# Kernel optimization log

Measured on AMD Instinct MI355X. Metric: run time of the kernel, lower is better.

The kernel has to match this reference:

```python
import jax, jax.numpy as jnp
import numpy as np

D = 256
NODE_COUNTS = [200000, 50000, 12000, 4000]  # n_src per block; dst of block l = NODE_COUNTS[l+1]
EDGE_COUNTS = [500000, 120000, 40000]


def setup_inputs() -> dict:
    key = jax.random.key(0)
    ks = jax.random.split(key, 16)
    x = jax.random.normal(ks[0], (NODE_COUNTS[0], D), dtype=jnp.float32)
    inp = {"x": x}
    scale = 1.0 / np.sqrt(D)
    ki = 1
    for l in range(3):
        inp[f"Wself{l}"] = jax.random.normal(ks[ki], (D, D), dtype=jnp.float32) * scale; ki += 1
        inp[f"Wneigh{l}"] = jax.random.normal(ks[ki], (D, D), dtype=jnp.float32) * scale; ki += 1
        inp[f"b{l}"] = jnp.zeros((D,), dtype=jnp.float32)
    for l in range(3):
        e = EDGE_COUNTS[l]
        inp[f"src{l}"] = jax.random.randint(ks[ki], (e,), 0, NODE_COUNTS[l]); ki += 1
        inp[f"dst{l}"] = jax.random.randint(ks[ki], (e,), 0, NODE_COUNTS[l + 1]); ki += 1
    inp["nd0"], inp["nd1"], inp["nd2"] = NODE_COUNTS[1], NODE_COUNTS[2], NODE_COUNTS[3]
    return inp


def _sage_layer(h, src, dst, n_dst, Ws, Wn, b, relu=True):
    # DGL SAGEConv('mean'): out = fc_self(h_dst) + fc_neigh(mean_{u in N(v)} h_u) + bias
    h_dst = h[:n_dst]
    msgs = h[src]                                               # [E, d] gather
    agg = jax.ops.segment_sum(msgs, dst, num_segments=n_dst)    # [n_dst, d]
    deg = jax.ops.segment_sum(jnp.ones((dst.shape[0],), h.dtype), dst, num_segments=n_dst)
    mean = agg / jnp.maximum(deg, 1.0)[:, None]
    out = h_dst @ Ws + mean @ Wn + b
    return jax.nn.relu(out) if relu else out


def reference(x, Wself0, Wneigh0, b0, Wself1, Wneigh1, b1, Wself2, Wneigh2, b2,
              src0, dst0, src1, dst1, src2, dst2, nd0, nd1, nd2):
    h = _sage_layer(x, src0, dst0, nd0, Wself0, Wneigh0, b0)
    h = _sage_layer(h, src1, dst1, nd1, Wself1, Wneigh1, b1)
    h = _sage_layer(h, src2, dst2, nd2, Wself2, Wneigh2, b2)
    return h
```

## Files before the change

kernel.cpp:

```cpp
#include <hip/hip_runtime.h>
#include <stdint.h>

#define D 256

typedef __attribute__((ext_vector_type(8))) short bf16x8;
typedef __attribute__((ext_vector_type(4))) float f32x4;

__device__ inline unsigned short f2bf(float f) {
    union { float f; uint32_t u; } v; v.f = f;
    return (unsigned short)((v.u + 0x7FFFu + ((v.u >> 16) & 1u)) >> 16);
}
__device__ inline float bf2f(unsigned short b) {
    return __uint_as_float(((uint32_t)b) << 16);
}

#define SEG0 0
#define SEG1 50176
#define SEG2 62464
#define CURTOT 66560
#define NBLK 65

#define WBLK 1536
#define XBLK 25000

struct PreArgs {
    const float* w[6];
    const float* x;
    unsigned short* wt;
    unsigned short* xb;
    const int* d0; const int* d1; const int* d2;
    int* cur;
    int E0, E01, Etot, cblk0;
};

__global__ __launch_bounds__(256) void fused_pre(PreArgs a)
{
    int b = blockIdx.x;
    if (b < WBLK) {
        int t = b * 256 + threadIdx.x;
        int m = t >> 16, e = t & 65535;
        int col = e >> 8, k = e & 255;
        a.wt[t] = f2bf(a.w[m][(k << 8) + col]);
    } else if (b < WBLK + XBLK) {
        long t = (long)(b - WBLK) * 256 + threadIdx.x;
        const float4* p = (const float4*)a.x + t * 2;
        float4 v0 = p[0], v1 = p[1];
        unsigned short r[8] = {f2bf(v0.x), f2bf(v0.y), f2bf(v0.z), f2bf(v0.w),
                               f2bf(v1.x), f2bf(v1.y), f2bf(v1.z), f2bf(v1.w)};
        *(uint4*)(a.xb + t * 8) = *(uint4*)r;
    } else {
        int e = (b - a.cblk0) * 256 + threadIdx.x;
        if (e >= a.Etot) return;
        int base, d;
        if (e < a.E0)       { base = SEG0; d = a.d0[e]; }
        else if (e < a.E01) { base = SEG1; d = a.d1[e - a.E0]; }
        else                { base = SEG2; d = a.d2[e - a.E01]; }
        atomicAdd(&a.cur[base + d], 1);
    }
}

__global__ __launch_bounds__(256) void scan_blocks(
    int* __restrict__ cur, int* __restrict__ bsum)
{
    __shared__ int wsum[4];
    int tid = threadIdx.x, lane = tid & 63, wid = tid >> 6;
    int base = blockIdx.x * 1024 + tid * 4;
    int4 v = *(int4*)(cur + base);
    int t0 = v.x, t01 = t0 + v.y, t012 = t01 + v.z, tot = t012 + v.w;
    int incl = tot;
    #pragma unroll
    for (int ofs = 1; ofs < 64; ofs <<= 1) {
        int t = __shfl_up(incl, ofs, 64);
        if (lane >= ofs) incl += t;
    }
    if (lane == 63) wsum[wid] = incl;
    __syncthreads();
    if (tid == 0) {
        int run = 0;
        #pragma unroll
        for (int w = 0; w < 4; ++w) { int t = wsum[w]; wsum[w] = run; run += t; }
        bsum[blockIdx.x] = run;
    }
    __syncthreads();
    int texcl = wsum[wid] + incl - tot;
    v.x = texcl; v.y = texcl + t0; v.z = texcl + t01; v.w = texcl + t012;
    *(int4*)(cur + base) = v;
}

__global__ __launch_bounds__(128) void scan_bsums(
    const int* __restrict__ bsum, int* __restrict__ bscan)
{
    __shared__ int s[NBLK];
    int tid = threadIdx.x;
    if (tid < NBLK) s[tid] = bsum[tid];
    __syncthreads();
    if (tid == 0) {
        int run = 0;
        for (int b = 0; b < 49; ++b)  { int t = s[b]; s[b] = run; run += t; }
        run = 0;
        for (int b = 49; b < 61; ++b) { int t = s[b]; s[b] = run; run += t; }
        run = 0;
        for (int b = 61; b < 65; ++b) { int t = s[b]; s[b] = run; run += t; }
    }
    __syncthreads();
    if (tid < NBLK) bscan[tid] = s[tid];
}

__global__ __launch_bounds__(256) void scan_addback(
    int* __restrict__ cur, const int* __restrict__ bscan)
{
    int base = blockIdx.x * 1024 + threadIdx.x * 4;
    int add = bscan[blockIdx.x];
    int4 v = *(int4*)(cur + base);
    v.x += add; v.y += add; v.z += add; v.w += add;
    *(int4*)(cur + base) = v;
}

__global__ __launch_bounds__(256) void fill_all(
    const int* __restrict__ s0, const int* __restrict__ s1, const int* __restrict__ s2,
    const int* __restrict__ d0, const int* __restrict__ d1, const int* __restrict__ d2,
    int* __restrict__ cur, int* __restrict__ idx, int E0, int E01, int Etot)
{
    int e = blockIdx.x * 256 + threadIdx.x;
    if (e >= Etot) return;
    int base, d, s, ib;
    if (e < E0)       { base = SEG0; d = d0[e];       s = s0[e];       ib = 0; }
    else if (e < E01) { base = SEG1; d = d1[e - E0];  s = s1[e - E0];  ib = E0; }
    else              { base = SEG2; d = d2[e - E01]; s = s2[e - E01]; ib = E01; }
    int p = atomicAdd(&cur[base + d], 1);
    idx[ib + p] = s;
}

__global__ __launch_bounds__(256) void gather_mean_k(
    const unsigned short* __restrict__ h, const int* __restrict__ idx,
    const int* __restrict__ curseg, unsigned short* __restrict__ mean, int M)
{
    int t = blockIdx.x * blockDim.x + threadIdx.x;
    int w = t >> 6, lane = t & 63;
    if (w >= M) return;
    int e0 = w ? curseg[w - 1] : 0;
    int e1 = curseg[w];
    float4 acc = make_float4(0.f, 0.f, 0.f, 0.f);
    int e = e0;
    for (; e + 1 < e1; e += 2) {
        int sa = idx[e], sb = idx[e + 1];
        ushort4 va = *(const ushort4*)(h + (size_t)sa * D + lane * 4);
        ushort4 vb = *(const ushort4*)(h + (size_t)sb * D + lane * 4);
        acc.x += bf2f(va.x) + bf2f(vb.x);
        acc.y += bf2f(va.y) + bf2f(vb.y);
        acc.z += bf2f(va.z) + bf2f(vb.z);
        acc.w += bf2f(va.w) + bf2f(vb.w);
    }
    if (e < e1) {
        int sa = idx[e];
        ushort4 va = *(const ushort4*)(h + (size_t)sa * D + lane * 4);
        acc.x += bf2f(va.x); acc.y += bf2f(va.y);
        acc.z += bf2f(va.z); acc.w += bf2f(va.w);
    }
    float r = 1.0f / fmaxf((float)(e1 - e0), 1.0f);
    ushort4 o;
    o.x = f2bf(acc.x * r); o.y = f2bf(acc.y * r);
    o.z = f2bf(acc.z * r); o.w = f2bf(acc.w * r);
    *(ushort4*)(mean + (size_t)w * D + lane * 4) = o;
}

template<int FINAL>
__global__ __launch_bounds__(256, 2) void sage_gemm_mfma(
    const unsigned short* __restrict__ A1,
    const unsigned short* __restrict__ A2,
    const unsigned short* __restrict__ Wt1,
    const unsigned short* __restrict__ Wt2,
    const float* __restrict__ bias,
    void* __restrict__ outv,
    int M)
{
    __shared__ unsigned short As[128 * 32];
    __shared__ unsigned short Bs[256 * 32];

    int tid = threadIdx.x;
    int lane = tid & 63, wid = tid >> 6;
    int wr = wid >> 1, wc = wid & 1;
    int m0 = blockIdx.x * 128;
    int l15 = lane & 15, lq = lane >> 4;

    f32x4 acc[4][8] = {};

    for (int kt = 0; kt < 16; ++kt) {
        const unsigned short* A = (kt < 8) ? A1 : A2;
        const unsigned short* B = (kt < 8) ? Wt1 : Wt2;
        int kk = (kt & 7) * 32;
        #pragma unroll
        for (int q = 0; q < 2; ++q) {
            int ch = q * 256 + tid;
            int r = ch >> 2, c16 = ch & 3;
            int gr = m0 + r; if (gr >= M) gr = M - 1;
            const unsigned short* src = A + (size_t)gr * 256 + kk + c16 * 8;
            __builtin_amdgcn_global_load_lds(
                (const __attribute__((address_space(1))) void*)src,
                (__attribute__((address_space(3))) void*)(As + (q * 256 + wid * 64) * 8),
                16, 0, 0);
        }
        #pragma unroll
        for (int q = 0; q < 4; ++q) {
            int ch = q * 256 + tid;
            int col = ch >> 2, c16 = ch & 3;
            const unsigned short* src = B + (size_t)col * 256 + kk + c16 * 8;
            __builtin_amdgcn_global_load_lds(
                (const __attribute__((address_space(1))) void*)src,
                (__attribute__((address_space(3))) void*)(Bs + (q * 256 + wid * 64) * 8),
                16, 0, 0);
        }
        __syncthreads();

        bf16x8 af[4], bfr[8];
        #pragma unroll
        for (int i = 0; i < 4; ++i)
            af[i] = *(const bf16x8*)(As + (wr * 64 + i * 16 + l15) * 32 + lq * 8);
        #pragma unroll
        for (int i = 0; i < 8; ++i)
            bfr[i] = *(const bf16x8*)(Bs + (wc * 128 + i * 16 + l15) * 32 + lq * 8);

        #pragma unroll
        for (int mr = 0; mr < 4; ++mr)
            #pragma unroll
            for (int nc = 0; nc < 8; ++nc)
                acc[mr][nc] = __builtin_amdgcn_mfma_f32_16x16x32_bf16(
                    af[mr], bfr[nc], acc[mr][nc], 0, 0, 0);
        __syncthreads();
    }

    #pragma unroll
    for (int nc = 0; nc < 8; ++nc) {
        int gc = wc * 128 + nc * 16 + l15;
        float bv = bias[gc];
        #pragma unroll
        for (int mr = 0; mr < 4; ++mr) {
            #pragma unroll
            for (int reg = 0; reg < 4; ++reg) {
                int gr = m0 + wr * 64 + mr * 16 + lq * 4 + reg;
                if (gr < M) {
                    float v = fmaxf(acc[mr][nc][reg] + bv, 0.f);
                    if (FINAL) ((float*)outv)[(size_t)gr * 256 + gc] = v;
                    else ((unsigned short*)outv)[(size_t)gr * 256 + gc] = f2bf(v);
                }
            }
        }
    }
}

extern "C" void kernel_launch(void* const* d_in, const int* in_sizes, int n_in,
                              void* d_out, int out_size, void* d_ws, size_t ws_size,
                              hipStream_t stream) {
    const float* x = (const float*)d_in[0];
    const float* Wself[3]  = {(const float*)d_in[1], (const float*)d_in[4], (const float*)d_in[7]};
    const float* Wneigh[3] = {(const float*)d_in[2], (const float*)d_in[5], (const float*)d_in[8]};
    const float* bias[3]   = {(const float*)d_in[3], (const float*)d_in[6], (const float*)d_in[9]};
    const int* src[3] = {(const int*)d_in[10], (const int*)d_in[12], (const int*)d_in[14]};
    const int* dst[3] = {(const int*)d_in[11], (const int*)d_in[13], (const int*)d_in[15]};
    int E[3]    = {in_sizes[10], in_sizes[12], in_sizes[14]};
    int ndst[3] = {50000, 12000, 4000};
    int E0 = E[0], E01 = E[0] + E[1], Etot = E[0] + E[1] + E[2];

    unsigned short* xb    = (unsigned short*)d_ws;
    unsigned short* h1b   = xb + (size_t)200000 * D;
    unsigned short* h2b   = h1b + (size_t)50000 * D;
    unsigned short* meanb = h2b + (size_t)12000 * D;
    unsigned short* wt    = meanb + (size_t)50000 * D;
    int* cur   = (int*)(wt + 6 * 65536);
    int* bsum  = cur + CURTOT;
    int* bscan = bsum + 80;
    int* idxa  = bscan + 80;

    hipMemsetAsync(cur, 0, CURTOT * sizeof(int), stream);

    PreArgs pa;
    pa.w[0] = Wself[0]; pa.w[1] = Wneigh[0];
    pa.w[2] = Wself[1]; pa.w[3] = Wneigh[1];
    pa.w[4] = Wself[2]; pa.w[5] = Wneigh[2];
    pa.x = x; pa.wt = wt; pa.xb = xb;
    pa.d0 = dst[0]; pa.d1 = dst[1]; pa.d2 = dst[2];
    pa.cur = cur; pa.E0 = E0; pa.E01 = E01; pa.Etot = Etot;
    pa.cblk0 = WBLK + XBLK;
    int cblk = (Etot + 255) / 256;
    fused_pre<<<WBLK + XBLK + cblk, 256, 0, stream>>>(pa);

    scan_blocks<<<NBLK, 256, 0, stream>>>(cur, bsum);
    scan_bsums<<<1, 128, 0, stream>>>(bsum, bscan);
    scan_addback<<<NBLK, 256, 0, stream>>>(cur, bscan);
    fill_all<<<(Etot + 255) / 256, 256, 0, stream>>>(src[0], src[1], src[2],
        dst[0], dst[1], dst[2], cur, idxa, E0, E01, Etot);

    const unsigned short* hin_b[3] = {xb, h1b, h2b};
    void* houts[3] = {h1b, h2b, d_out};
    int segb[3] = {SEG0, SEG1, SEG2};
    int idxb[3] = {0, E0, E01};

    for (int l = 0; l < 3; ++l) {
        int M = ndst[l];
        int gt = M * 64;
        gather_mean_k<<<(gt + 255) / 256, 256, 0, stream>>>(
            hin_b[l], idxa + idxb[l], cur + segb[l], meanb, M);

        dim3 grid((M + 127) / 128);
        if (l < 2)
            sage_gemm_mfma<0><<<grid, 256, 0, stream>>>(hin_b[l], meanb,
                wt + (size_t)(2 * l) * 65536, wt + (size_t)(2 * l + 1) * 65536,
                bias[l], houts[l], M);
        else
            sage_gemm_mfma<1><<<grid, 256, 0, stream>>>(hin_b[l], meanb,
                wt + (size_t)(2 * l) * 65536, wt + (size_t)(2 * l + 1) * 65536,
                bias[l], houts[l], M);
    }
}
```

Before: 308.2 us.

## Fuse neighbor gather-mean into GEMM, drop x bf16 pass, single-pass lookback scan

```diff
diff --git a/kernel.cpp b/kernel.cpp
--- a/kernel.cpp
+++ b/kernel.cpp
@@ -13,6 +13,8 @@
 __device__ inline float bf2f(unsigned short b) {
     return __uint_as_float(((uint32_t)b) << 16);
 }
+__device__ inline float bflo(unsigned int u) { return __uint_as_float(u << 16); }
+__device__ inline float bfhi(unsigned int u) { return __uint_as_float(u & 0xffff0000u); }
 
 #define SEG0 0
 #define SEG1 50176
@@ -21,16 +23,13 @@
 #define NBLK 65
 
 #define WBLK 1536
-#define XBLK 25000
 
 struct PreArgs {
     const float* w[6];
-    const float* x;
     unsigned short* wt;
-    unsigned short* xb;
     const int* d0; const int* d1; const int* d2;
     int* cur;
-    int E0, E01, Etot, cblk0;
+    int E0, E01, Etot;
 };
 
 __global__ __launch_bounds__(256) void fused_pre(PreArgs a)
@@ -41,15 +40,8 @@
         int m = t >> 16, e = t & 65535;
         int col = e >> 8, k = e & 255;
         a.wt[t] = f2bf(a.w[m][(k << 8) + col]);
-    } else if (b < WBLK + XBLK) {
-        long t = (long)(b - WBLK) * 256 + threadIdx.x;
-        const float4* p = (const float4*)a.x + t * 2;
-        float4 v0 = p[0], v1 = p[1];
-        unsigned short r[8] = {f2bf(v0.x), f2bf(v0.y), f2bf(v0.z), f2bf(v0.w),
-                               f2bf(v1.x), f2bf(v1.y), f2bf(v1.z), f2bf(v1.w)};
-        *(uint4*)(a.xb + t * 8) = *(uint4*)r;
     } else {
-        int e = (b - a.cblk0) * 256 + threadIdx.x;
+        int e = (b - WBLK) * 256 + threadIdx.x;
         if (e >= a.Etot) return;
         int base, d;
         if (e < a.E0)       { base = SEG0; d = a.d0[e]; }
@@ -59,12 +51,14 @@
     }
 }
 
-__global__ __launch_bounds__(256) void scan_blocks(
-    int* __restrict__ cur, int* __restrict__ bsum)
+__global__ __launch_bounds__(256) void scan_lookback(
+    int* __restrict__ cur, unsigned int* __restrict__ flag)
 {
     __shared__ int wsum[4];
+    __shared__ int sprefix;
     int tid = threadIdx.x, lane = tid & 63, wid = tid >> 6;
-    int base = blockIdx.x * 1024 + tid * 4;
+    int b = blockIdx.x;
+    int base = b * 1024 + tid * 4;
     int4 v = *(int4*)(cur + base);
     int t0 = v.x, t01 = t0 + v.y, t012 = t01 + v.z, tot = t012 + v.w;
     int incl = tot;
@@ -79,40 +73,23 @@
         int run = 0;
         #pragma unroll
         for (int w = 0; w < 4; ++w) { int t = wsum[w]; wsum[w] = run; run += t; }
-        bsum[blockIdx.x] = run;
+        int segfirst = (b >= 61) ? 61 : (b >= 49) ? 49 : 0;
+        int pfx = 0;
+        if (b != segfirst) {
+            unsigned int f;
+            do {
+                f = __hip_atomic_load(&flag[b - 1], __ATOMIC_ACQUIRE,
+                                      __HIP_MEMORY_SCOPE_AGENT);
+            } while (f == 0);
+            pfx = (int)(f - 1u);
+        }
+        __hip_atomic_store(&flag[b], (unsigned int)(pfx + run) + 1u,
+                           __ATOMIC_RELEASE, __HIP_MEMORY_SCOPE_AGENT);
+        sprefix = pfx;
     }
     __syncthreads();
-    int texcl = wsum[wid] + incl - tot;
-    v.x = texcl; v.y = texcl + t0; v.z = texcl + t01; v.w = texcl + t012;
-    *(int4*)(cur + base) = v;
-}
-
-__global__ __launch_bounds__(128) void scan_bsums(
-    const int* __restrict__ bsum, int* __restrict__ bscan)
-{
-    __shared__ int s[NBLK];
-    int tid = threadIdx.x;
-    if (tid < NBLK) s[tid] = bsum[tid];
-    __syncthreads();
-    if (tid == 0) {
-        int run = 0;
-        for (int b = 0; b < 49; ++b)  { int t = s[b]; s[b] = run; run += t; }
-        run = 0;
-        for (int b = 49; b < 61; ++b) { int t = s[b]; s[b] = run; run += t; }
-        run = 0;
-        for (int b = 61; b < 65; ++b) { int t = s[b]; s[b] = run; run += t; }
-    }
-    __syncthreads();
-    if (tid < NBLK) bscan[tid] = s[tid];
-}
-
-__global__ __launch_bounds__(256) void scan_addback(
-    int* __restrict__ cur, const int* __restrict__ bscan)
-{
-    int base = blockIdx.x * 1024 + threadIdx.x * 4;
-    int add = bscan[blockIdx.x];
-    int4 v = *(int4*)(cur + base);
-    v.x += add; v.y += add; v.z += add; v.w += add;
+    int add = sprefix + wsum[wid] + incl - tot;
+    v.x = add; v.y = add + t0; v.z = add + t01; v.w = add + t012;
     *(int4*)(cur + base) = v;
 }
 
@@ -131,43 +108,11 @@
     idx[ib + p] = s;
 }
 
-__global__ __launch_bounds__(256) void gather_mean_k(
-    const unsigned short* __restrict__ h, const int* __restrict__ idx,
-    const int* __restrict__ curseg, unsigned short* __restrict__ mean, int M)
-{
-    int t = blockIdx.x * blockDim.x + threadIdx.x;
-    int w = t >> 6, lane = t & 63;
-    if (w >= M) return;
-    int e0 = w ? curseg[w - 1] : 0;
-    int e1 = curseg[w];
-    float4 acc = make_float4(0.f, 0.f, 0.f, 0.f);
-    int e = e0;
-    for (; e + 1 < e1; e += 2) {
-        int sa = idx[e], sb = idx[e + 1];
-        ushort4 va = *(const ushort4*)(h + (size_t)sa * D + lane * 4);
-        ushort4 vb = *(const ushort4*)(h + (size_t)sb * D + lane * 4);
-        acc.x += bf2f(va.x) + bf2f(vb.x);
-        acc.y += bf2f(va.y) + bf2f(vb.y);
-        acc.z += bf2f(va.z) + bf2f(vb.z);
-        acc.w += bf2f(va.w) + bf2f(vb.w);
-    }
-    if (e < e1) {
-        int sa = idx[e];
-        ushort4 va = *(const ushort4*)(h + (size_t)sa * D + lane * 4);
-        acc.x += bf2f(va.x); acc.y += bf2f(va.y);
-        acc.z += bf2f(va.z); acc.w += bf2f(va.w);
-    }
-    float r = 1.0f / fmaxf((float)(e1 - e0), 1.0f);
-    ushort4 o;
-    o.x = f2bf(acc.x * r); o.y = f2bf(acc.y * r);
-    o.z = f2bf(acc.z * r); o.w = f2bf(acc.w * r);
-    *(ushort4*)(mean + (size_t)w * D + lane * 4) = o;
-}
-
-template<int FINAL>
-__global__ __launch_bounds__(256, 2) void sage_gemm_mfma(
-    const unsigned short* __restrict__ A1,
-    const unsigned short* __restrict__ A2,
+template<int FINAL, int F32>
+__global__ __launch_bounds__(512) void sage_fused(
+    const void* __restrict__ hv,
+    const int* __restrict__ idx,
+    const int* __restrict__ curseg,
     const unsigned short* __restrict__ Wt1,
     const unsigned short* __restrict__ Wt2,
     const float* __restrict__ bias,
@@ -179,59 +124,117 @@
 
     int tid = threadIdx.x;
     int lane = tid & 63, wid = tid >> 6;
-    int wr = wid >> 1, wc = wid & 1;
+    int wr = wid >> 2, wc = wid & 3;
     int m0 = blockIdx.x * 128;
     int l15 = lane & 15, lq = lane >> 4;
 
-    f32x4 acc[4][8] = {};
+    int ar = tid >> 2, ac = tid & 3;
+    int w = m0 + ar; if (w >= M) w = M - 1;
+    int e0 = w ? curseg[w - 1] : 0;
+    int e1 = curseg[w];
+    float rdeg = 1.0f / fmaxf((float)(e1 - e0), 1.0f);
+
+    f32x4 acc[4][4] = {};
 
     for (int kt = 0; kt < 16; ++kt) {
-        const unsigned short* A = (kt < 8) ? A1 : A2;
+        int kk = (kt & 7) * 32;
         const unsigned short* B = (kt < 8) ? Wt1 : Wt2;
-        int kk = (kt & 7) * 32;
         #pragma unroll
         for (int q = 0; q < 2; ++q) {
-            int ch = q * 256 + tid;
-            int r = ch >> 2, c16 = ch & 3;
-            int gr = m0 + r; if (gr >= M) gr = M - 1;
-            const unsigned short* src = A + (size_t)gr * 256 + kk + c16 * 8;
+            int ch = q * 512 + tid;
+            int col = ch >> 2, c = ch & 3;
+            const unsigned short* s = B + (size_t)col * 256 + kk + c * 8;
             __builtin_amdgcn_global_load_lds(
-                (const __attribute__((address_space(1))) void*)src,
-                (__attribute__((address_space(3))) void*)(As + (q * 256 + wid * 64) * 8),
+                (const __attribute__((address_space(1))) void*)s,
+                (__attribute__((address_space(3))) void*)(Bs + ch * 8),
                 16, 0, 0);
         }
-        #pragma unroll
-        for (int q = 0; q < 4; ++q) {
-            int ch = q * 256 + tid;
-            int col = ch >> 2, c16 = ch & 3;
-            const unsigned short* src = B + (size_t)col * 256 + kk + c16 * 8;
-            __builtin_amdgcn_global_load_lds(
-                (const __attribute__((address_space(1))) void*)src,
-                (__attribute__((address_space(3))) void*)(Bs + (q * 256 + wid * 64) * 8),
-                16, 0, 0);
+        if (kt < 8) {
+            if (F32) {
+                const float* h = (const float*)hv;
+                const float* s = h + (size_t)w * 256 + kk + ac * 8;
+                float4 u0 = *(const float4*)s;
+                float4 u1 = *(const float4*)(s + 4);
+                unsigned short rr[8] = {f2bf(u0.x), f2bf(u0.y), f2bf(u0.z), f2bf(u0.w),
+                                        f2bf(u1.x), f2bf(u1.y), f2bf(u1.z), f2bf(u1.w)};
+                *(uint4*)(As + tid * 8) = *(uint4*)rr;
+            } else {
+                const unsigned short* h = (const unsigned short*)hv;
+                const unsigned short* s = h + (size_t)w * 256 + kk + ac * 8;
+                __builtin_amdgcn_global_load_lds(
+                    (const __attribute__((address_space(1))) void*)s,
+                    (__attribute__((address_space(3))) void*)(As + tid * 8),
+                    16, 0, 0);
+            }
+        } else {
+            float a0 = 0.f, a1 = 0.f, a2 = 0.f, a3 = 0.f,
+                  a4 = 0.f, a5 = 0.f, a6 = 0.f, a7 = 0.f;
+            if (F32) {
+                const float* h = (const float*)hv;
+                int e = e0;
+                for (; e + 1 < e1; e += 2) {
+                    int sa = idx[e], sb = idx[e + 1];
+                    const float* pa = h + (size_t)sa * 256 + kk + ac * 8;
+                    const float* pb = h + (size_t)sb * 256 + kk + ac * 8;
+                    float4 x0 = *(const float4*)pa, x1 = *(const float4*)(pa + 4);
+                    float4 y0 = *(const float4*)pb, y1 = *(const float4*)(pb + 4);
+                    a0 += x0.x + y0.x; a1 += x0.y + y0.y;
+                    a2 += x0.z + y0.z; a3 += x0.w + y0.w;
+                    a4 += x1.x + y1.x; a5 += x1.y + y1.y;
+                    a6 += x1.z + y1.z; a7 += x1.w + y1.w;
+                }
+                if (e < e1) {
+                    const float* pa = h + (size_t)idx[e] * 256 + kk + ac * 8;
+                    float4 x0 = *(const float4*)pa, x1 = *(const float4*)(pa + 4);
+                    a0 += x0.x; a1 += x0.y; a2 += x0.z; a3 += x0.w;
+                    a4 += x1.x; a5 += x1.y; a6 += x1.z; a7 += x1.w;
+                }
+            } else {
+                const unsigned short* h = (const unsigned short*)hv;
+                int e = e0;
+                for (; e + 1 < e1; e += 2) {
+                    int sa = idx[e], sb = idx[e + 1];
+                    uint4 u = *(const uint4*)(h + (size_t)sa * 256 + kk + ac * 8);
+                    uint4 v = *(const uint4*)(h + (size_t)sb * 256 + kk + ac * 8);
+                    a0 += bflo(u.x) + bflo(v.x); a1 += bfhi(u.x) + bfhi(v.x);
+                    a2 += bflo(u.y) + bflo(v.y); a3 += bfhi(u.y) + bfhi(v.y);
+                    a4 += bflo(u.z) + bflo(v.z); a5 += bfhi(u.z) + bfhi(v.z);
+                    a6 += bflo(u.w) + bflo(v.w); a7 += bfhi(u.w) + bfhi(v.w);
+                }
+                if (e < e1) {
+                    uint4 u = *(const uint4*)(h + (size_t)idx[e] * 256 + kk + ac * 8);
+                    a0 += bflo(u.x); a1 += bfhi(u.x);
+                    a2 += bflo(u.y); a3 += bfhi(u.y);
+                    a4 += bflo(u.z); a5 += bfhi(u.z);
+                    a6 += bflo(u.w); a7 += bfhi(u.w);
+                }
+            }
+            unsigned short rr[8] = {f2bf(a0 * rdeg), f2bf(a1 * rdeg),
+                                    f2bf(a2 * rdeg), f2bf(a3 * rdeg),
+                                    f2bf(a4 * rdeg), f2bf(a5 * rdeg),
+                                    f2bf(a6 * rdeg), f2bf(a7 * rdeg)};
+            *(uint4*)(As + tid * 8) = *(uint4*)rr;
         }
         __syncthreads();
 
-        bf16x8 af[4], bfr[8];
-        #pragma unroll
-        for (int i = 0; i < 4; ++i)
-            af[i] = *(const bf16x8*)(As + (wr * 64 + i * 16 + l15) * 32 + lq * 8);
-        #pragma unroll
-        for (int i = 0; i < 8; ++i)
-            bfr[i] = *(const bf16x8*)(Bs + (wc * 128 + i * 16 + l15) * 32 + lq * 8);
-
+        bf16x8 af[4], bfr[4];
+        #pragma unroll
+        for (int i = 0; i < 4; ++i) {
+            af[i]  = *(const bf16x8*)(As + (wr * 64 + i * 16 + l15) * 32 + lq * 8);
+            bfr[i] = *(const bf16x8*)(Bs + (wc * 64 + i * 16 + l15) * 32 + lq * 8);
+        }
         #pragma unroll
         for (int mr = 0; mr < 4; ++mr)
             #pragma unroll
-            for (int nc = 0; nc < 8; ++nc)
+            for (int nc = 0; nc < 4; ++nc)
                 acc[mr][nc] = __builtin_amdgcn_mfma_f32_16x16x32_bf16(
                     af[mr], bfr[nc], acc[mr][nc], 0, 0, 0);
         __syncthreads();
     }
 
     #pragma unroll
-    for (int nc = 0; nc < 8; ++nc) {
-        int gc = wc * 128 + nc * 16 + l15;
+    for (int nc = 0; nc < 4; ++nc) {
+        int gc = wc * 64 + nc * 16 + l15;
         float bv = bias[gc];
         #pragma unroll
         for (int mr = 0; mr < 4; ++mr) {
@@ -261,54 +264,37 @@
     int ndst[3] = {50000, 12000, 4000};
     int E0 = E[0], E01 = E[0] + E[1], Etot = E[0] + E[1] + E[2];
 
-    unsigned short* xb    = (unsigned short*)d_ws;
-    unsigned short* h1b   = xb + (size_t)200000 * D;
-    unsigned short* h2b   = h1b + (size_t)50000 * D;
-    unsigned short* meanb = h2b + (size_t)12000 * D;
-    unsigned short* wt    = meanb + (size_t)50000 * D;
-    int* cur   = (int*)(wt + 6 * 65536);
-    int* bsum  = cur + CURTOT;
-    int* bscan = bsum + 80;
-    int* idxa  = bscan + 80;
-
-    hipMemsetAsync(cur, 0, CURTOT * sizeof(int), stream);
+    unsigned short* h1b = (unsigned short*)d_ws;
+    unsigned short* h2b = h1b + (size_t)50000 * D;
+    unsigned short* wt  = h2b + (size_t)12000 * D;
+    int* cur            = (int*)(wt + 6 * 65536);
+    unsigned int* flag  = (unsigned int*)(cur + CURTOT);
+    int* idxa           = (int*)(flag + 80);
+
+    hipMemsetAsync(cur, 0, (CURTOT + 80) * sizeof(int), stream);
 
     PreArgs pa;
     pa.w[0] = Wself[0]; pa.w[1] = Wneigh[0];
     pa.w[2] = Wself[1]; pa.w[3] = Wneigh[1];
     pa.w[4] = Wself[2]; pa.w[5] = Wneigh[2];
-    pa.x = x; pa.wt = wt; pa.xb = xb;
+    pa.wt = wt;
     pa.d0 = dst[0]; pa.d1 = dst[1]; pa.d2 = dst[2];
     pa.cur = cur; pa.E0 = E0; pa.E01 = E01; pa.Etot = Etot;
-    pa.cblk0 = WBLK + XBLK;
     int cblk = (Etot + 255) / 256;
-    fused_pre<<<WBLK + XBLK + cblk, 256, 0, stream>>>(pa);
-
-    scan_blocks<<<NBLK, 256, 0, stream>>>(cur, bsum);
-    scan_bsums<<<1, 128, 0, stream>>>(bsum, bscan);
-    scan_addback<<<NBLK, 256, 0, stream>>>(cur, bscan);
+    fused_pre<<<WBLK + cblk, 256, 0, stream>>>(pa);
+
+    scan_lookback<<<NBLK, 256, 0, stream>>>(cur, flag);
+
     fill_all<<<(Etot + 255) / 256, 256, 0, stream>>>(src[0], src[1], src[2],
         dst[0], dst[1], dst[2], cur, idxa, E0, E01, Etot);
 
-    const unsigned short* hin_b[3] = {xb, h1b, h2b};
-    void* houts[3] = {h1b, h2b, d_out};
-    int segb[3] = {SEG0, SEG1, SEG2};
-    int idxb[3] = {0, E0, E01};
-
-    for (int l = 0; l < 3; ++l) {
-        int M = ndst[l];
-        int gt = M * 64;
-        gather_mean_k<<<(gt + 255) / 256, 256, 0, stream>>>(
-            hin_b[l], idxa + idxb[l], cur + segb[l], meanb, M);
-
-        dim3 grid((M + 127) / 128);
-        if (l < 2)
-            sage_gemm_mfma<0><<<grid, 256, 0, stream>>>(hin_b[l], meanb,
-                wt + (size_t)(2 * l) * 65536, wt + (size_t)(2 * l + 1) * 65536,
-                bias[l], houts[l], M);
-        else
-            sage_gemm_mfma<1><<<grid, 256, 0, stream>>>(hin_b[l], meanb,
-                wt + (size_t)(2 * l) * 65536, wt + (size_t)(2 * l + 1) * 65536,
-                bias[l], houts[l], M);
-    }
-}
+    sage_fused<0, 1><<<(50000 + 127) / 128, 512, 0, stream>>>(
+        x, idxa + 0, cur + SEG0, wt + 0 * 65536, wt + 1 * 65536,
+        bias[0], h1b, 50000);
+    sage_fused<0, 0><<<(12000 + 127) / 128, 512, 0, stream>>>(
+        h1b, idxa + E0, cur + SEG1, wt + 2 * 65536, wt + 3 * 65536,
+        bias[1], h2b, 12000);
+    sage_fused<1, 0><<<(4000 + 127) / 128, 512, 0, stream>>>(
+        h2b, idxa + E01, cur + SEG2, wt + 4 * 65536, wt + 5 * 65536,
+        bias[2], d_out, 4000);
+}
```

New measurement: 420.7 us. +36.5%, slower.
